# Kernel tuning notes

Hardware: AMD Instinct MI355X
Metric: run time of the kernel (lower is better)

The kernel has to match this reference:

```python
import jax, jax.numpy as jnp
import numpy as np

NUM_LAYERS = 3  # min_num_layers == max_num_layers == 3 (deterministic stochastic depth)
LN_EPS = 1e-5


def setup_inputs() -> dict:
    key = jax.random.key(0)
    k1, k2, k3 = jax.random.split(key, 3)
    N, d, F = 8, 16, 512  # (batch, in_dim=out_dim, num_features)
    x = jax.random.normal(k1, (N, d, F), dtype=jnp.float32)
    W = jax.random.normal(k2, (d, F, F, d), dtype=jnp.float32)  # recurrent weight
    A = jax.random.uniform(k3, (2, F, F), dtype=jnp.float32)    # transition mats, steps 1..2
    return {"x": x, "W": W, "A": A}


def _contract(h, W, a):
    # h: (N,d,F), W: (d,F,F,o), a: (F,F) -> (N,o,F)
    # Equivalent to (h.unsqueeze(-1).unsqueeze(-1) * (W * a[...,None])).sum(1).sum(1).transpose(1,2)
    return jnp.einsum('ndf,dfgo,fg->nog', h, W, a)


def _layer_norm(y):
    # torch applies layer_norm over the channel dim (axis 1 of (N,o,F)), no affine params
    m = y.mean(axis=1, keepdims=True)
    v = y.var(axis=1, keepdims=True)
    return (y - m) / jnp.sqrt(v + LN_EPS)


def reference(x, W, A):
    history = [x]
    for i in range(1, NUM_LAYERS):
        # recurrent + residual branch: average contributions from all previous layers
        ys = [_contract(history[j], W, A[i - j - 1]) for j in range(i)]
        y = jnp.mean(jnp.stack(ys, axis=0), axis=0)
        y = _layer_norm(y)
        history.append(y)
    return history[-1]  # return_layers='last'
```

## Files before the change

### kernel.cpp

```cpp
#include <hip/hip_runtime.h>
#include <stdint.h>


#define FC  8
#define NCH 64

__global__ void k0_prep_x(const float* __restrict__ x, float* __restrict__ xT) {
    int idx = blockIdx.x * blockDim.x + threadIdx.x;
    int n = idx & 7, d = (idx >> 3) & 15, f = idx >> 7;
    xT[idx] = x[n * 8192 + d * 512 + f];
}

template <bool PASS_A>
__global__ __launch_bounds__(256)
void k_contract(const float* __restrict__ W, const float* __restrict__ A,
                const float* __restrict__ xT,
                float* __restrict__ p0, float* __restrict__ p1) {
    const int t   = threadIdx.x;
    const int fc  = blockIdx.x;
    const int ct  = blockIdx.y;
    const int col = ct * 256 + t;
    const int g   = col >> 4;
    const int f0  = fc * FC;

    const float* Wc = W + col;

    float c0[8], c1[8];
#pragma unroll
    for (int n = 0; n < 8; ++n) { c0[n] = 0.f; c1[n] = 0.f; }

    float w[16], wn[16];
    {
        const int f_first = PASS_A ? f0 : (f0 + FC - 1);
#pragma unroll
        for (int d = 0; d < 16; ++d)
            w[d] = Wc[(size_t)d * 4194304 + (size_t)f_first * 8192];
    }

#pragma unroll
    for (int ff = 0; ff < FC; ++ff) {
        const int f  = PASS_A ? (f0 + ff) : (f0 + FC - 1 - ff);
        const int fn = PASS_A ? (f + 1) : (f - 1);

        if (ff + 1 < FC) {
#pragma unroll
            for (int d = 0; d < 16; ++d)
                wn[d] = Wc[(size_t)d * 4194304 + (size_t)fn * 8192];
        }

        float a0 = A[f * 512 + g];
        float a1 = 0.f;
        if constexpr (PASS_A) a1 = A[262144 + f * 512 + g];

        const float* xf = xT + f * 128;
        float p[8];
#pragma unroll
        for (int n = 0; n < 8; ++n) p[n] = 0.f;
#pragma unroll
        for (int d = 0; d < 16; ++d) {
#pragma unroll
            for (int n = 0; n < 8; ++n)
                p[n] = fmaf(xf[d * 8 + n], w[d], p[n]);
        }

#pragma unroll
        for (int n = 0; n < 8; ++n) c0[n] = fmaf(a0, p[n], c0[n]);
        if constexpr (PASS_A) {
#pragma unroll
            for (int n = 0; n < 8; ++n) c1[n] = fmaf(a1, p[n], c1[n]);
        }

        if (ff + 1 < FC) {
#pragma unroll
            for (int d = 0; d < 16; ++d) w[d] = wn[d];
        }
    }

    float4* dst0 = reinterpret_cast<float4*>(p0 + ((size_t)fc * 8192 + col) * 8);
    dst0[0] = make_float4(c0[0], c0[1], c0[2], c0[3]);
    dst0[1] = make_float4(c0[4], c0[5], c0[6], c0[7]);
    if constexpr (PASS_A) {
        float4* dst1 = reinterpret_cast<float4*>(p1 + ((size_t)fc * 8192 + col) * 8);
        dst1[0] = make_float4(c1[0], c1[1], c1[2], c1[3]);
        dst1[1] = make_float4(c1[4], c1[5], c1[6], c1[7]);
    }
}

__global__ __launch_bounds__(128)
void k_reduce_ln(const float* __restrict__ part, float* __restrict__ outT) {
    __shared__ float sh[16][8];
    int g = blockIdx.x;
    int t = threadIdx.x;
    int o = t >> 3, n = t & 7;
    size_t base = ((size_t)g * 16 + o) * 8 + n;
    float s0 = 0.f, s1 = 0.f, s2 = 0.f, s3 = 0.f;
#pragma unroll
    for (int ch = 0; ch < NCH; ch += 4) {
        s0 += part[(size_t)(ch + 0) * 65536 + base];
        s1 += part[(size_t)(ch + 1) * 65536 + base];
        s2 += part[(size_t)(ch + 2) * 65536 + base];
        s3 += part[(size_t)(ch + 3) * 65536 + base];
    }
    float s = (s0 + s1) + (s2 + s3);
    sh[o][n] = s;
    __syncthreads();
    float m = 0.f, v = 0.f;
#pragma unroll
    for (int oo = 0; oo < 16; ++oo) { float y = sh[oo][n]; m += y; v += y * y; }
    m *= (1.f / 16.f);
    v = v * (1.f / 16.f) - m * m;
    float r = rsqrtf(v + 1e-5f);
    outT[base] = (s - m) * r;
}

__global__ __launch_bounds__(128)
void k_final(const float* __restrict__ p1, const float* __restrict__ p2,
             float* __restrict__ out) {
    __shared__ float sh[16][8];
    int g = blockIdx.x;
    int t = threadIdx.x;
    int o = t >> 3, n = t & 7;
    size_t base = ((size_t)g * 16 + o) * 8 + n;
    float s0 = 0.f, s1 = 0.f, s2 = 0.f, s3 = 0.f;
#pragma unroll
    for (int ch = 0; ch < NCH; ch += 2) {
        size_t i0 = (size_t)(ch + 0) * 65536 + base;
        size_t i1 = (size_t)(ch + 1) * 65536 + base;
        s0 += p1[i0]; s1 += p2[i0];
        s2 += p1[i1]; s3 += p2[i1];
    }
    float s = 0.5f * ((s0 + s1) + (s2 + s3));
    sh[o][n] = s;
    __syncthreads();
    float m = 0.f, v = 0.f;
#pragma unroll
    for (int oo = 0; oo < 16; ++oo) { float y = sh[oo][n]; m += y; v += y * y; }
    m *= (1.f / 16.f);
    v = v * (1.f / 16.f) - m * m;
    float r = rsqrtf(v + 1e-5f);
    out[n * 8192 + o * 512 + g] = (s - m) * r;
}

extern "C" void kernel_launch(void* const* d_in, const int* in_sizes, int n_in,
                              void* d_out, int out_size, void* d_ws, size_t ws_size,
                              hipStream_t stream) {
    const float* x = (const float*)d_in[0];
    const float* W = (const float*)d_in[1];
    const float* A = (const float*)d_in[2];
    float* out = (float*)d_out;

    float* ws  = (float*)d_ws;
    float* xT  = ws;
    float* xT2 = ws + 65536;
    float* c0p = ws + 131072;
    float* c1p = c0p + 4194304;
    float* c2p = c1p + 4194304;

    k0_prep_x<<<256, 256, 0, stream>>>(x, xT);
    k_contract<true ><<<dim3(NCH, 32), 256, 0, stream>>>(W, A, xT,  c0p, c1p);
    k_reduce_ln<<<512, 128, 0, stream>>>(c0p, xT2);
    k_contract<false><<<dim3(NCH, 32), 256, 0, stream>>>(W, A, xT2, c2p, nullptr);
    k_final<<<512, 128, 0, stream>>>(c1p, c2p, out);
}
```

Baseline: 459.4 us.

## Process four W columns per thread with float4 loads and shared x/A tiles

Each thread of the contraction kernel now handles four adjacent output columns, loading W with float4 vector loads. The grid shrinks fourfold to match. The per-block slices of x and A are staged once in shared memory instead of being read from global memory on every step. The explicit double-buffered prefetch of W is dropped in favour of straight vector loads. This raises register pressure (a 4x8 accumulator set) and leaves fewer blocks to hide memory latency on what is a bandwidth-bound stream over the 268MB W tensor.

```diff
diff --git a/kernel.cpp b/kernel.cpp
--- a/kernel.cpp
+++ b/kernel.cpp
@@ -2,8 +2,8 @@
 #include <stdint.h>
 
 
-#define FC  8
-#define NCH 64
+#define FC   8
+#define NFCH 64
 
 __global__ void k0_prep_x(const float* __restrict__ x, float* __restrict__ xT) {
     int idx = blockIdx.x * blockDim.x + threadIdx.x;
@@ -16,73 +16,102 @@
 void k_contract(const float* __restrict__ W, const float* __restrict__ A,
                 const float* __restrict__ xT,
                 float* __restrict__ p0, float* __restrict__ p1) {
+    __shared__ float sx[FC][16][8];
+    __shared__ float sA[2][FC][64];
+
     const int t   = threadIdx.x;
     const int fc  = blockIdx.x;
-    const int ct  = blockIdx.y;
-    const int col = ct * 256 + t;
-    const int g   = col >> 4;
+    const int cg  = blockIdx.y;
     const int f0  = fc * FC;
+    const int col = cg * 1024 + t * 4;
+    const int gl  = t >> 2;
+
+    {
+        const float4* src = reinterpret_cast<const float4*>(xT + (size_t)f0 * 128);
+        reinterpret_cast<float4*>(&sx[0][0][0])[t] = src[t];
+    }
+    {
+        int fl = t >> 5, gg = (t & 31) * 2;
+        *reinterpret_cast<float2*>(&sA[0][fl][gg]) =
+            *reinterpret_cast<const float2*>(&A[(size_t)(f0 + fl) * 512 + cg * 64 + gg]);
+        if constexpr (PASS_A)
+            *reinterpret_cast<float2*>(&sA[1][fl][gg]) =
+                *reinterpret_cast<const float2*>(&A[262144 + (size_t)(f0 + fl) * 512 + cg * 64 + gg]);
+    }
+    __syncthreads();
 
     const float* Wc = W + col;
 
-    float c0[8], c1[8];
+    float c0[4][8], c1[4][8];
 #pragma unroll
-    for (int n = 0; n < 8; ++n) { c0[n] = 0.f; c1[n] = 0.f; }
-
-    float w[16], wn[16];
-    {
-        const int f_first = PASS_A ? f0 : (f0 + FC - 1);
+    for (int c = 0; c < 4; ++c)
 #pragma unroll
-        for (int d = 0; d < 16; ++d)
-            w[d] = Wc[(size_t)d * 4194304 + (size_t)f_first * 8192];
-    }
+        for (int n = 0; n < 8; ++n) { c0[c][n] = 0.f; c1[c][n] = 0.f; }
 
 #pragma unroll
     for (int ff = 0; ff < FC; ++ff) {
-        const int f  = PASS_A ? (f0 + ff) : (f0 + FC - 1 - ff);
-        const int fn = PASS_A ? (f + 1) : (f - 1);
+        const int fl = PASS_A ? ff : (FC - 1 - ff);
+        const int f  = f0 + fl;
 
-        if (ff + 1 < FC) {
+        float4 w[16];
 #pragma unroll
-            for (int d = 0; d < 16; ++d)
-                wn[d] = Wc[(size_t)d * 4194304 + (size_t)fn * 8192];
+        for (int d = 0; d < 16; ++d)
+            w[d] = *reinterpret_cast<const float4*>(
+                Wc + (size_t)d * 4194304 + (size_t)f * 8192);
+
+        float p[4][8];
+#pragma unroll
+        for (int c = 0; c < 4; ++c)
+#pragma unroll
+            for (int n = 0; n < 8; ++n) p[c][n] = 0.f;
+
+#pragma unroll
+        for (int d = 0; d < 16; ++d) {
+            float4 xa = *reinterpret_cast<const float4*>(&sx[fl][d][0]);
+            float4 xb = *reinterpret_cast<const float4*>(&sx[fl][d][4]);
+#define FMA8(c, wc) \
+            p[c][0] = fmaf(xa.x, wc, p[c][0]); \
+            p[c][1] = fmaf(xa.y, wc, p[c][1]); \
+            p[c][2] = fmaf(xa.z, wc, p[c][2]); \
+            p[c][3] = fmaf(xa.w, wc, p[c][3]); \
+            p[c][4] = fmaf(xb.x, wc, p[c][4]); \
+            p[c][5] = fmaf(xb.y, wc, p[c][5]); \
+            p[c][6] = fmaf(xb.z, wc, p[c][6]); \
+            p[c][7] = fmaf(xb.w, wc, p[c][7]);
+            FMA8(0, w[d].x)
+            FMA8(1, w[d].y)
+            FMA8(2, w[d].z)
+            FMA8(3, w[d].w)
+#undef FMA8
         }
 
-        float a0 = A[f * 512 + g];
-        float a1 = 0.f;
-        if constexpr (PASS_A) a1 = A[262144 + f * 512 + g];
-
-        const float* xf = xT + f * 128;
-        float p[8];
+        const float a0 = sA[0][fl][gl];
 #pragma unroll
-        for (int n = 0; n < 8; ++n) p[n] = 0.f;
+        for (int c = 0; c < 4; ++c)
 #pragma unroll
-        for (int d = 0; d < 16; ++d) {
+            for (int n = 0; n < 8; ++n) c0[c][n] = fmaf(a0, p[c][n], c0[c][n]);
+        if constexpr (PASS_A) {
+            const float a1 = sA[1][fl][gl];
 #pragma unroll
-            for (int n = 0; n < 8; ++n)
-                p[n] = fmaf(xf[d * 8 + n], w[d], p[n]);
-        }
-
+            for (int c = 0; c < 4; ++c)
 #pragma unroll
-        for (int n = 0; n < 8; ++n) c0[n] = fmaf(a0, p[n], c0[n]);
-        if constexpr (PASS_A) {
-#pragma unroll
-            for (int n = 0; n < 8; ++n) c1[n] = fmaf(a1, p[n], c1[n]);
-        }
-
-        if (ff + 1 < FC) {
-#pragma unroll
-            for (int d = 0; d < 16; ++d) w[d] = wn[d];
+                for (int n = 0; n < 8; ++n) c1[c][n] = fmaf(a1, p[c][n], c1[c][n]);
         }
     }
 
     float4* dst0 = reinterpret_cast<float4*>(p0 + ((size_t)fc * 8192 + col) * 8);
-    dst0[0] = make_float4(c0[0], c0[1], c0[2], c0[3]);
-    dst0[1] = make_float4(c0[4], c0[5], c0[6], c0[7]);
+#pragma unroll
+    for (int c = 0; c < 4; ++c) {
+        dst0[2 * c + 0] = make_float4(c0[c][0], c0[c][1], c0[c][2], c0[c][3]);
+        dst0[2 * c + 1] = make_float4(c0[c][4], c0[c][5], c0[c][6], c0[c][7]);
+    }
     if constexpr (PASS_A) {
         float4* dst1 = reinterpret_cast<float4*>(p1 + ((size_t)fc * 8192 + col) * 8);
-        dst1[0] = make_float4(c1[0], c1[1], c1[2], c1[3]);
-        dst1[1] = make_float4(c1[4], c1[5], c1[6], c1[7]);
+#pragma unroll
+        for (int c = 0; c < 4; ++c) {
+            dst1[2 * c + 0] = make_float4(c1[c][0], c1[c][1], c1[c][2], c1[c][3]);
+            dst1[2 * c + 1] = make_float4(c1[c][4], c1[c][5], c1[c][6], c1[c][7]);
+        }
     }
 }
 
@@ -95,7 +124,7 @@
     size_t base = ((size_t)g * 16 + o) * 8 + n;
     float s0 = 0.f, s1 = 0.f, s2 = 0.f, s3 = 0.f;
 #pragma unroll
-    for (int ch = 0; ch < NCH; ch += 4) {
+    for (int ch = 0; ch < NFCH; ch += 4) {
         s0 += part[(size_t)(ch + 0) * 65536 + base];
         s1 += part[(size_t)(ch + 1) * 65536 + base];
         s2 += part[(size_t)(ch + 2) * 65536 + base];
@@ -123,7 +152,7 @@
     size_t base = ((size_t)g * 16 + o) * 8 + n;
     float s0 = 0.f, s1 = 0.f, s2 = 0.f, s3 = 0.f;
 #pragma unroll
-    for (int ch = 0; ch < NCH; ch += 2) {
+    for (int ch = 0; ch < NFCH; ch += 2) {
         size_t i0 = (size_t)(ch + 0) * 65536 + base;
         size_t i1 = (size_t)(ch + 1) * 65536 + base;
         s0 += p1[i0]; s1 += p2[i0];
@@ -157,8 +186,8 @@
     float* c2p = c1p + 4194304;
 
     k0_prep_x<<<256, 256, 0, stream>>>(x, xT);
-    k_contract<true ><<<dim3(NCH, 32), 256, 0, stream>>>(W, A, xT,  c0p, c1p);
+    k_contract<true ><<<dim3(NFCH, 8), 256, 0, stream>>>(W, A, xT,  c0p, c1p);
     k_reduce_ln<<<512, 128, 0, stream>>>(c0p, xT2);
-    k_contract<false><<<dim3(NCH, 32), 256, 0, stream>>>(W, A, xT2, c2p, nullptr);
+    k_contract<false><<<dim3(NFCH, 8), 256, 0, stream>>>(W, A, xT2, c2p, nullptr);
     k_final<<<512, 128, 0, stream>>>(c1p, c2p, out);
 }
```

Result: slower. 507.7 us (+10.5%).

## Restructure contraction to split over d-groups and f-slices with shared-memory staging

Applied to the files above, without the earlier changes.

The contraction kernel now splits work over f-slices of 32 and d-groups of 2, with 512-thread blocks. Each thread handles 4 contiguous columns through float4 W loads, and x and A are staged in shared memory. A is folded into W before the FMAs, replacing the per-d inner product. This yields 128 partial slices instead of 64, which doubles the partial-buffer traffic in the reduce kernels, and the second pass reuses the first partial buffer. The intent is wider, better coalesced W streaming and less redundant global loading of A and x.

```diff
diff --git a/kernel.cpp b/kernel.cpp
--- a/kernel.cpp
+++ b/kernel.cpp
@@ -2,8 +2,11 @@
 #include <stdint.h>
 
 
-#define FC  8
-#define NCH 64
+#define FS   32
+#define NFS  16
+#define DPG  2
+#define NDG  8
+#define NSL  128
 
 __global__ void k0_prep_x(const float* __restrict__ x, float* __restrict__ xT) {
     int idx = blockIdx.x * blockDim.x + threadIdx.x;
@@ -12,77 +15,97 @@
 }
 
 template <bool PASS_A>
-__global__ __launch_bounds__(256)
+__global__ __launch_bounds__(512)
 void k_contract(const float* __restrict__ W, const float* __restrict__ A,
                 const float* __restrict__ xT,
                 float* __restrict__ p0, float* __restrict__ p1) {
-    const int t   = threadIdx.x;
-    const int fc  = blockIdx.x;
-    const int ct  = blockIdx.y;
-    const int col = ct * 256 + t;
-    const int g   = col >> 4;
-    const int f0  = fc * FC;
+    __shared__ float sx[DPG][FS][8];
+    __shared__ float sA[2][FS][128];
 
-    const float* Wc = W + col;
+    const int t  = threadIdx.x;
+    const int fs = blockIdx.x;
+    const int cq = blockIdx.y;
+    const int dg = blockIdx.z;
+    const int f0 = fs * FS;
 
-    float c0[8], c1[8];
+    {
+        int dd = t >> 8, fl = (t >> 3) & 31, n = t & 7;
+        sx[dd][fl][n] = xT[(size_t)(f0 + fl) * 128 + (dg * DPG + dd) * 8 + n];
+    }
+    {
+        int gl = (t & 31) * 4, flb = t >> 5;
 #pragma unroll
-    for (int n = 0; n < 8; ++n) { c0[n] = 0.f; c1[n] = 0.f; }
+        for (int k = 0; k < 2; ++k) {
+            int fl = flb + k * 16;
+            *reinterpret_cast<float4*>(&sA[0][fl][gl]) =
+                *reinterpret_cast<const float4*>(&A[(size_t)(f0 + fl) * 512 + cq * 128 + gl]);
+            if constexpr (PASS_A)
+                *reinterpret_cast<float4*>(&sA[1][fl][gl]) =
+                    *reinterpret_cast<const float4*>(&A[262144 + (size_t)(f0 + fl) * 512 + cq * 128 + gl]);
+        }
+    }
+    __syncthreads();
 
-    float w[16], wn[16];
-    {
-        const int f_first = PASS_A ? f0 : (f0 + FC - 1);
+    const int gl   = t >> 2;
+    const int col4 = cq * 2048 + t * 4;
+
+    float c0[4][8], c1[4][8];
 #pragma unroll
-        for (int d = 0; d < 16; ++d)
-            w[d] = Wc[(size_t)d * 4194304 + (size_t)f_first * 8192];
-    }
+    for (int c = 0; c < 4; ++c)
+#pragma unroll
+        for (int n = 0; n < 8; ++n) { c0[c][n] = 0.f; c1[c][n] = 0.f; }
 
+    const float* Wbase = W + (size_t)(dg * DPG) * 4194304 + (size_t)f0 * 8192 + col4;
 #pragma unroll
-    for (int ff = 0; ff < FC; ++ff) {
-        const int f  = PASS_A ? (f0 + ff) : (f0 + FC - 1 - ff);
-        const int fn = PASS_A ? (f + 1) : (f - 1);
+    for (int dd = 0; dd < DPG; ++dd) {
+        const float* Wd = Wbase + (size_t)dd * 4194304;
+#pragma unroll 4
+        for (int fl = 0; fl < FS; ++fl) {
+            float4 w  = *reinterpret_cast<const float4*>(Wd + (size_t)fl * 8192);
+            float4 xa = *reinterpret_cast<const float4*>(&sx[dd][fl][0]);
+            float4 xb = *reinterpret_cast<const float4*>(&sx[dd][fl][4]);
 
-        if (ff + 1 < FC) {
-#pragma unroll
-            for (int d = 0; d < 16; ++d)
-                wn[d] = Wc[(size_t)d * 4194304 + (size_t)fn * 8192];
-        }
-
-        float a0 = A[f * 512 + g];
-        float a1 = 0.f;
-        if constexpr (PASS_A) a1 = A[262144 + f * 512 + g];
-
-        const float* xf = xT + f * 128;
-        float p[8];
-#pragma unroll
-        for (int n = 0; n < 8; ++n) p[n] = 0.f;
-#pragma unroll
-        for (int d = 0; d < 16; ++d) {
-#pragma unroll
-            for (int n = 0; n < 8; ++n)
-                p[n] = fmaf(xf[d * 8 + n], w[d], p[n]);
-        }
-
-#pragma unroll
-        for (int n = 0; n < 8; ++n) c0[n] = fmaf(a0, p[n], c0[n]);
-        if constexpr (PASS_A) {
-#pragma unroll
-            for (int n = 0; n < 8; ++n) c1[n] = fmaf(a1, p[n], c1[n]);
-        }
-
-        if (ff + 1 < FC) {
-#pragma unroll
-            for (int d = 0; d < 16; ++d) w[d] = wn[d];
+            float a0 = sA[0][fl][gl];
+            float4 w0 = make_float4(w.x * a0, w.y * a0, w.z * a0, w.w * a0);
+#define FMA8(acc, c, wc) \
+            acc[c][0] = fmaf(xa.x, wc, acc[c][0]); \
+            acc[c][1] = fmaf(xa.y, wc, acc[c][1]); \
+            acc[c][2] = fmaf(xa.z, wc, acc[c][2]); \
+            acc[c][3] = fmaf(xa.w, wc, acc[c][3]); \
+            acc[c][4] = fmaf(xb.x, wc, acc[c][4]); \
+            acc[c][5] = fmaf(xb.y, wc, acc[c][5]); \
+            acc[c][6] = fmaf(xb.z, wc, acc[c][6]); \
+            acc[c][7] = fmaf(xb.w, wc, acc[c][7]);
+            FMA8(c0, 0, w0.x)
+            FMA8(c0, 1, w0.y)
+            FMA8(c0, 2, w0.z)
+            FMA8(c0, 3, w0.w)
+            if constexpr (PASS_A) {
+                float a1 = sA[1][fl][gl];
+                float4 w1 = make_float4(w.x * a1, w.y * a1, w.z * a1, w.w * a1);
+                FMA8(c1, 0, w1.x)
+                FMA8(c1, 1, w1.y)
+                FMA8(c1, 2, w1.z)
+                FMA8(c1, 3, w1.w)
+            }
+#undef FMA8
         }
     }
 
-    float4* dst0 = reinterpret_cast<float4*>(p0 + ((size_t)fc * 8192 + col) * 8);
-    dst0[0] = make_float4(c0[0], c0[1], c0[2], c0[3]);
-    dst0[1] = make_float4(c0[4], c0[5], c0[6], c0[7]);
+    const int s = dg * NFS + fs;
+    float* d0 = p0 + (size_t)s * 65536 + (size_t)col4 * 8;
+#pragma unroll
+    for (int c = 0; c < 4; ++c) {
+        *reinterpret_cast<float4*>(d0 + c * 8 + 0) = make_float4(c0[c][0], c0[c][1], c0[c][2], c0[c][3]);
+        *reinterpret_cast<float4*>(d0 + c * 8 + 4) = make_float4(c0[c][4], c0[c][5], c0[c][6], c0[c][7]);
+    }
     if constexpr (PASS_A) {
-        float4* dst1 = reinterpret_cast<float4*>(p1 + ((size_t)fc * 8192 + col) * 8);
-        dst1[0] = make_float4(c1[0], c1[1], c1[2], c1[3]);
-        dst1[1] = make_float4(c1[4], c1[5], c1[6], c1[7]);
+        float* d1 = p1 + (size_t)s * 65536 + (size_t)col4 * 8;
+#pragma unroll
+        for (int c = 0; c < 4; ++c) {
+            *reinterpret_cast<float4*>(d1 + c * 8 + 0) = make_float4(c1[c][0], c1[c][1], c1[c][2], c1[c][3]);
+            *reinterpret_cast<float4*>(d1 + c * 8 + 4) = make_float4(c1[c][4], c1[c][5], c1[c][6], c1[c][7]);
+        }
     }
 }
 
@@ -95,7 +118,7 @@
     size_t base = ((size_t)g * 16 + o) * 8 + n;
     float s0 = 0.f, s1 = 0.f, s2 = 0.f, s3 = 0.f;
 #pragma unroll
-    for (int ch = 0; ch < NCH; ch += 4) {
+    for (int ch = 0; ch < NSL; ch += 4) {
         s0 += part[(size_t)(ch + 0) * 65536 + base];
         s1 += part[(size_t)(ch + 1) * 65536 + base];
         s2 += part[(size_t)(ch + 2) * 65536 + base];
@@ -123,7 +146,7 @@
     size_t base = ((size_t)g * 16 + o) * 8 + n;
     float s0 = 0.f, s1 = 0.f, s2 = 0.f, s3 = 0.f;
 #pragma unroll
-    for (int ch = 0; ch < NCH; ch += 2) {
+    for (int ch = 0; ch < NSL; ch += 2) {
         size_t i0 = (size_t)(ch + 0) * 65536 + base;
         size_t i1 = (size_t)(ch + 1) * 65536 + base;
         s0 += p1[i0]; s1 += p2[i0];
@@ -153,12 +176,12 @@
     float* xT  = ws;
     float* xT2 = ws + 65536;
     float* c0p = ws + 131072;
-    float* c1p = c0p + 4194304;
-    float* c2p = c1p + 4194304;
+    float* c1p = c0p + 8388608;
+    float* c2p = c0p;
 
     k0_prep_x<<<256, 256, 0, stream>>>(x, xT);
-    k_contract<true ><<<dim3(NCH, 32), 256, 0, stream>>>(W, A, xT,  c0p, c1p);
+    k_contract<true ><<<dim3(NFS, 4, NDG), 512, 0, stream>>>(W, A, xT,  c0p, c1p);
     k_reduce_ln<<<512, 128, 0, stream>>>(c0p, xT2);
-    k_contract<false><<<dim3(NCH, 32), 256, 0, stream>>>(W, A, xT2, c2p, nullptr);
+    k_contract<false><<<dim3(NFS, 4, NDG), 512, 0, stream>>>(W, A, xT2, c2p, nullptr);
     k_final<<<512, 128, 0, stream>>>(c1p, c2p, out);
 }
```

Result: no change. 464.0 us (+1.0%).
